# Kernel optimization log

Measured on AMD Instinct MI355X. Metric: run time of the kernel, lower is better.

## Reference

```python
import jax, jax.numpy as jnp
import numpy as np

B, N, IN, OUT, H = 256, 131, 512, 1024, 4
D = OUT // H  # head_dim
EDGE_SCALE = D ** -0.5
NODE_SCALE = OUT ** -0.5

lrelu = lambda x: jax.nn.leaky_relu(x, negative_slope=0.01)


def _glorot(key, shape):
    fan_in = shape[-1]
    return jax.random.normal(key, shape, dtype=jnp.float32) * (1.0 / np.sqrt(fan_in))


def setup_inputs() -> dict:
    key = jax.random.key(0)
    ks = jax.random.split(key, 16)
    return {
        "tabular_feats": jax.random.normal(ks[0], (B, 1, IN), dtype=jnp.float32),
        "node_feats": jax.random.normal(ks[1], (B, N, IN), dtype=jnp.float32),
        "adj_matrix": jax.random.uniform(ks[2], (B, N, N), dtype=jnp.float32),
        "W_gx": _glorot(ks[3], (OUT, IN)), "b_gx": jnp.zeros((OUT,), jnp.float32),
        "W_tx": _glorot(ks[4], (OUT, IN)), "b_tx": jnp.zeros((OUT,), jnp.float32),
        "W_gk": _glorot(ks[5], (OUT, IN)),
        "W_tq": _glorot(ks[6], (OUT, IN)),
        "W_gq": _glorot(ks[7], (OUT, IN)),
        "W_gs": _glorot(ks[8], (1, N)), "b_gs": jnp.zeros((1,), jnp.float32),
        "W_zx": _glorot(ks[9], (OUT, 2 * OUT)), "b_zx": jnp.zeros((OUT,), jnp.float32),
    }


def preprocess_adj(A):
    # add self-loops then symmetric degree normalization D^{-1/2} (A+I) D^{-1/2}
    A = A + jnp.eye(A.shape[-1], dtype=A.dtype)
    d_inv = jax.lax.rsqrt(jnp.sum(A, axis=-1))  # [b,h,x]
    return d_inv[..., :, None] * A * d_inv[..., None, :]


def reference(tabular_feats, node_feats, adj_matrix,
              W_gx, b_gx, W_tx, b_tx, W_gk, W_tq, W_gq, W_gs, b_gs, W_zx, b_zx):
    G_X = lrelu(node_feats @ W_gx.T + b_gx)            # [B,N,OUT]
    T_X = lrelu(tabular_feats @ W_tx.T + b_tx)         # [B,1,OUT]
    G_k = lrelu(node_feats @ W_gk.T)                   # [B,N,OUT]
    T_q = lrelu(tabular_feats @ W_tq.T)                # [B,1,OUT]

    node_att = jax.nn.softmax(jnp.einsum('bxh,byh->bxy', T_q, G_k) * NODE_SCALE, axis=-1)
    node_att = jnp.swapaxes(node_att + 1.0, -1, -2)    # [B,N,1]
    G_X = node_att * G_X                               # [B,N,OUT]

    G_X_mh = G_X.reshape(B, N, H, D).transpose(0, 2, 1, 3)            # [B,H,N,D]
    G_q_mh = lrelu(node_feats @ W_gq.T).reshape(B, N, H, D).transpose(0, 2, 1, 3)
    G_k_mh = G_k.reshape(B, N, H, D).transpose(0, 2, 1, 3)

    edge_att = jax.nn.sigmoid(jnp.einsum('bhxd,bhyd->bhxy', G_q_mh, G_k_mh) * EDGE_SCALE)
    adj_heads = adj_matrix[:, None] * edge_att         # [B,H,N,N]
    A = preprocess_adj(adj_heads)

    G_X = jnp.einsum('bhxy,bhyd->bhxd', A, G_X_mh).transpose(0, 2, 1, 3).reshape(B, N, OUT)

    # Graph_summary: Linear(num_node -> 1) over the node axis
    global_node = lrelu(jnp.einsum('bno,n->bo', G_X, W_gs[0]) + b_gs)  # [B,OUT]
    Z_in = jnp.concatenate([global_node, T_X.reshape(B, -1)], axis=-1)  # [B,2*OUT]
    Z_x = lrelu(Z_in @ W_zx.T + b_zx)                  # [B,OUT]
    return (G_X, T_X, Z_x, node_att, edge_att)
```

## Files before the change

kernel.cpp:

```cpp
#include <hip/hip_runtime.h>
#include <hip/hip_bf16.h>
#include <math.h>


#define LRELU(x) ((x) > 0.f ? (x) : 0.01f * (x))

constexpr int Bb = 256;
constexpr int Nn = 131;
constexpr int INF_ = 512;
constexpr int OUTF = 1024;
constexpr int Hh = 4;
constexpr int Dd = 256;
constexpr int OC2 = 2048;
constexpr int YP = 168;
constexpr int WLP = 174;
constexpr int KAGG = 160;

typedef __attribute__((ext_vector_type(8))) short bf16x8;
typedef __attribute__((ext_vector_type(4))) float f32x4;

__device__ __forceinline__ float bf2f(short s) {
    union { float f; unsigned u; } c;
    c.u = ((unsigned)(unsigned short)s) << 16;
    return c.f;
}

__device__ __forceinline__ void gload_lds16(const void* g, void* lds) {
    __builtin_amdgcn_global_load_lds(
        (const __attribute__((address_space(1))) void*)g,
        (__attribute__((address_space(3))) void*)lds, 16, 0, 0);
}

__global__ __launch_bounds__(256) void convert_kernel(
    const float* __restrict__ node, const float* __restrict__ Wgx,
    const float* __restrict__ Wgk, const float* __restrict__ Wgq,
    __hip_bfloat16* __restrict__ node_bf, __hip_bfloat16* __restrict__ Wcat)
{
    const size_t NE = (size_t)Bb * Nn * INF_ / 4;
    const size_t WE = (size_t)3072 * INF_ / 4;
    for (size_t i = (size_t)blockIdx.x * 256 + threadIdx.x; i < NE + WE;
         i += (size_t)gridDim.x * 256) {
        if (i < NE) {
            const float4 v = ((const float4*)node)[i];
            __hip_bfloat16* o = node_bf + i * 4;
            o[0] = __float2bfloat16(v.x); o[1] = __float2bfloat16(v.y);
            o[2] = __float2bfloat16(v.z); o[3] = __float2bfloat16(v.w);
        } else {
            const size_t j = i - NE;
            const size_t which = j / (1024 * INF_ / 4);
            const float* src = (which == 0) ? Wgk : (which == 1 ? Wgq : Wgx);
            const size_t srcj = j - which * (1024 * INF_ / 4);
            const float4 v = ((const float4*)src)[srcj];
            __hip_bfloat16* o = Wcat + j * 4;
            o[0] = __float2bfloat16(v.x); o[1] = __float2bfloat16(v.y);
            o[2] = __float2bfloat16(v.z); o[3] = __float2bfloat16(v.w);
        }
    }
}

__global__ __launch_bounds__(256, 4) void gemm_node_mfma(
    const __hip_bfloat16* __restrict__ A, const __hip_bfloat16* __restrict__ W,
    const float* __restrict__ bias_gx, const float* __restrict__ Tq,
    __hip_bfloat16* __restrict__ Gcat, __hip_bfloat16* __restrict__ GrawT,
    float* __restrict__ spart)
{
    __shared__ short SM[16384];
    short* As = SM;
    short* Bs = SM + 8192;
    const int tid = threadIdx.x;
    const int wave = tid >> 6, lane = tid & 63;
    const int m0 = blockIdx.y * 128, o0 = blockIdx.x * 128;
    const int wr = wave >> 1, wc = wave & 1;

    f32x4 acc[4][4] = {};
    const short* Asrc = (const short*)A;
    const short* Wsrc = (const short*)W;
    const int gsrc = ((tid & 7) ^ ((tid >> 3) & 7)) * 8;
    const int srow = tid >> 3;

    for (int kt = 0; kt < 8; ++kt) {
        const int k0 = kt * 64;
        #pragma unroll
        for (int j = 0; j < 4; ++j) {
            const int row = j * 32 + srow;
            gload_lds16(Asrc + (size_t)(m0 + row) * INF_ + k0 + gsrc,
                        &As[(j * 256 + (tid & ~63)) * 8]);
            gload_lds16(Wsrc + (size_t)(o0 + row) * INF_ + k0 + gsrc,
                        &Bs[(j * 256 + (tid & ~63)) * 8]);
        }
        __syncthreads();
        #pragma unroll
        for (int ks = 0; ks < 2; ++ks) {
            const int sa = ((ks * 4 + (lane >> 4)) ^ (lane & 7)) * 8;
            bf16x8 af[4], bfr[4];
            #pragma unroll
            for (int i = 0; i < 4; ++i) {
                af[i]  = *(const bf16x8*)&As[(wr * 64 + i * 16 + (lane & 15)) * 64 + sa];
                bfr[i] = *(const bf16x8*)&Bs[(wc * 64 + i * 16 + (lane & 15)) * 64 + sa];
            }
            #pragma unroll
            for (int mi = 0; mi < 4; ++mi)
                #pragma unroll
                for (int ni = 0; ni < 4; ++ni)
                    acc[mi][ni] = __builtin_amdgcn_mfma_f32_16x16x32_bf16(
                        af[mi], bfr[ni], acc[mi][ni], 0, 0, 0);
        }
        __syncthreads();
    }

    const int cc = lane & 15;
    const int rg = (lane >> 4) * 4;
    if (o0 < 1024) {
        const int blo = m0 / 131;
        const int msw = (blo + 1) * 131;
        float tqA[4], tqB[4];
        #pragma unroll
        for (int ni = 0; ni < 4; ++ni) {
            const int o = o0 + wc * 64 + ni * 16 + cc;
            tqA[ni] = Tq[(size_t)blo * OUTF + o];
            tqB[ni] = (blo + 1 < Bb) ? Tq[(size_t)(blo + 1) * OUTF + o] : 0.f;
        }
        float sc[4][4] = {};
        #pragma unroll
        for (int mi = 0; mi < 4; ++mi)
            #pragma unroll
            for (int ni = 0; ni < 4; ++ni) {
                const int o = o0 + wc * 64 + ni * 16 + cc;
                #pragma unroll
                for (int r = 0; r < 4; ++r) {
                    const int m = m0 + wr * 64 + mi * 16 + rg + r;
                    float v = acc[mi][ni][r];
                    v = LRELU(v);
                    Gcat[(size_t)m * OC2 + o] = __float2bfloat16(v);
                    sc[mi][r] += v * ((m >= msw) ? tqB[ni] : tqA[ni]);
                }
            }
        const int slot = (o0 >> 6) + wc;
        #pragma unroll
        for (int mi = 0; mi < 4; ++mi)
            #pragma unroll
            for (int r = 0; r < 4; ++r) {
                float s = sc[mi][r];
                s += __shfl_xor(s, 1); s += __shfl_xor(s, 2);
                s += __shfl_xor(s, 4); s += __shfl_xor(s, 8);
                if (cc == 0) {
                    const int m = m0 + wr * 64 + mi * 16 + rg + r;
                    spart[(size_t)m * 16 + slot] = s;
                }
            }
    } else if (o0 < OC2) {
        #pragma unroll
        for (int mi = 0; mi < 4; ++mi)
            #pragma unroll
            for (int ni = 0; ni < 4; ++ni) {
                const int o = o0 + wc * 64 + ni * 16 + cc;
                #pragma unroll
                for (int r = 0; r < 4; ++r) {
                    const int m = m0 + wr * 64 + mi * 16 + rg + r;
                    float v = acc[mi][ni][r];
                    v = LRELU(v);
                    Gcat[(size_t)m * OC2 + o] = __float2bfloat16(v);
                }
            }
    } else {
        const int og0 = o0 - OC2;
        const int h = og0 >> 8;
        const int dbase = og0 & 255;
        __syncthreads();
        #pragma unroll
        for (int mi = 0; mi < 4; ++mi)
            #pragma unroll
            for (int ni = 0; ni < 4; ++ni) {
                const int dloc = wc * 64 + ni * 16 + cc;
                const float badd = bias_gx[og0 + dloc];
                #pragma unroll
                for (int r = 0; r < 4; ++r) {
                    const int row = wr * 64 + mi * 16 + rg + r;
                    float v = acc[mi][ni][r] + badd;
                    v = LRELU(v);
                    __hip_bfloat16 hb = __float2bfloat16(v);
                    const int g = row >> 3;
                    SM[dloc * 128 + ((g ^ (dloc & 7)) << 3) + (row & 7)] = *(short*)&hb;
                }
            }
        __syncthreads();
        short* GT = (short*)GrawT;
        #pragma unroll
        for (int j = 0; j < 8; ++j) {
            const int task = j * 256 + tid;
            const int dloc = task >> 4;
            const int g = task & 15;
            const bf16x8 v = *(const bf16x8*)&SM[dloc * 128 + ((g ^ (dloc & 7)) << 3)];
            const int m = m0 + g * 8;
            const int gd = dbase + dloc;
            const int b0 = m / 131;
            const int n0 = m - b0 * 131;
            if (n0 + 8 <= Nn) {
                *(bf16x8*)&GT[((size_t)(b0 * Hh + h) * 256 + gd) * YP + n0] = v;
            } else {
                #pragma unroll
                for (int e = 0; e < 8; ++e) {
                    const int mm = m + e;
                    const int bb = mm / 131;
                    const int nn = mm - bb * 131;
                    GT[((size_t)(bb * Hh + h) * 256 + gd) * YP + nn] = ((const short*)&v)[e];
                }
            }
        }
    }
}

__global__ __launch_bounds__(256) void gemm_tab(
    const float* __restrict__ Atab, const float* __restrict__ Wtx,
    const float* __restrict__ btx, const float* __restrict__ Wtq,
    float* __restrict__ Ctx, float* __restrict__ Ctq)
{
    const int which = blockIdx.x >> 4;
    const float* Wm = which ? Wtq : Wtx;
    float* C = which ? Ctq : Ctx;
    __shared__ float As[16][68];
    __shared__ float Ws[16][68];
    const int tid = threadIdx.x;
    const int tx = tid & 15;
    const int ty = tid >> 4;
    const int m0 = blockIdx.y * 64;
    const int o0 = (blockIdx.x & 15) * 64;

    float acc[4][4] = {};
    for (int k0 = 0; k0 < INF_; k0 += 16) {
        const int j = tid & 15;
        const int i = tid >> 4;
        #pragma unroll
        for (int r = 0; r < 4; ++r)
            As[j][i + 16 * r] = Atab[(size_t)(m0 + i + 16 * r) * INF_ + k0 + j];
        #pragma unroll
        for (int r = 0; r < 4; ++r)
            Ws[j][i + 16 * r] = Wm[(size_t)(o0 + i + 16 * r) * INF_ + k0 + j];
        __syncthreads();
        #pragma unroll
        for (int kk = 0; kk < 16; ++kk) {
            const float4 av = *(const float4*)&As[kk][ty * 4];
            const float4 wv = *(const float4*)&Ws[kk][tx * 4];
            const float a[4] = {av.x, av.y, av.z, av.w};
            const float w[4] = {wv.x, wv.y, wv.z, wv.w};
            #pragma unroll
            for (int r = 0; r < 4; ++r)
                #pragma unroll
                for (int c = 0; c < 4; ++c)
                    acc[r][c] += a[r] * w[c];
        }
        __syncthreads();
    }
    #pragma unroll
    for (int r = 0; r < 4; ++r) {
        const int m = m0 + ty * 4 + r;
        const int o = o0 + tx * 4;
        float4 v;
        float* vp = (float*)&v;
        #pragma unroll
        for (int c = 0; c < 4; ++c) {
            float t = acc[r][c] + (which ? 0.f : btx[o + c]);
            vp[c] = LRELU(t);
        }
        *(float4*)&C[(size_t)m * OUTF + o] = v;
    }
}

__global__ __launch_bounds__(256) void zin_build(
    const float* __restrict__ gnode, const float* __restrict__ bgs,
    const float* __restrict__ Tx, float* __restrict__ Zin)
{
    const int idx = blockIdx.x * 256 + threadIdx.x;
    const int b = idx >> 10, o = idx & 1023;
    const float s = gnode[idx] + bgs[0];
    Zin[(size_t)b * 2048 + o] = LRELU(s);
    Zin[(size_t)b * 2048 + 1024 + o] = Tx[idx];
}

__global__ __launch_bounds__(256) void gemm_zsplit(
    const float* __restrict__ A, const float* __restrict__ W,
    float* __restrict__ P)
{
    __shared__ float As[16][68];
    __shared__ float Ws[16][68];
    const int tid = threadIdx.x;
    const int tx = tid & 15;
    const int ty = tid >> 4;
    const int m0 = blockIdx.y * 64;
    const int o0 = blockIdx.x * 64;
    const int kbase = blockIdx.z * 512;

    float acc[4][4] = {};
    for (int k0 = kbase; k0 < kbase + 512; k0 += 16) {
        const int j = tid & 15;
        const int i = tid >> 4;
        #pragma unroll
        for (int r = 0; r < 4; ++r)
            As[j][i + 16 * r] = A[(size_t)(m0 + i + 16 * r) * 2048 + k0 + j];
        #pragma unroll
        for (int r = 0; r < 4; ++r)
            Ws[j][i + 16 * r] = W[(size_t)(o0 + i + 16 * r) * 2048 + k0 + j];
        __syncthreads();
        #pragma unroll
        for (int kk = 0; kk < 16; ++kk) {
            const float4 av = *(const float4*)&As[kk][ty * 4];
            const float4 wv = *(const float4*)&Ws[kk][tx * 4];
            const float a[4] = {av.x, av.y, av.z, av.w};
            const float w[4] = {wv.x, wv.y, wv.z, wv.w};
            #pragma unroll
            for (int r = 0; r < 4; ++r)
                #pragma unroll
                for (int c = 0; c < 4; ++c)
                    acc[r][c] += a[r] * w[c];
        }
        __syncthreads();
    }
    float* pz = P + (size_t)blockIdx.z * Bb * OUTF;
    #pragma unroll
    for (int r = 0; r < 4; ++r) {
        const int m = m0 + ty * 4 + r;
        const int o = o0 + tx * 4;
        float4 v;
        float* vp = (float*)&v;
        #pragma unroll
        for (int c = 0; c < 4; ++c) vp[c] = acc[r][c];
        *(float4*)&pz[(size_t)m * OUTF + o] = v;
    }
}

__global__ __launch_bounds__(256) void zreduce(
    const float* __restrict__ P, const float* __restrict__ bzx,
    float* __restrict__ C)
{
    const int idx = blockIdx.x * 256 + threadIdx.x;
    const int o = idx & 1023;
    const size_t STRIDE = (size_t)Bb * OUTF;
    float s = P[idx] + P[STRIDE + idx] + P[2 * STRIDE + idx] + P[3 * STRIDE + idx]
            + bzx[o];
    C[idx] = LRELU(s);
}

__global__ __launch_bounds__(256) void nodeatt_soft(
    const float* __restrict__ spart, float* __restrict__ att)
{
    const int b = blockIdx.x;
    __shared__ float sc[136];
    const int tid = threadIdx.x;
    if (tid < Nn) {
        const float* sp = spart + (size_t)(b * Nn + tid) * 16;
        float s = 0.f;
        #pragma unroll
        for (int i = 0; i < 16; ++i) s += sp[i];
        sc[tid] = s * (1.f / 32.f);
    }
    __syncthreads();
    if (tid < 64) {
        const float v1 = sc[tid];
        const float v2 = sc[tid + 64];
        const float v3 = (tid < 3) ? sc[tid + 128] : -1e30f;
        float m = fmaxf(fmaxf(v1, v2), v3);
        #pragma unroll
        for (int off = 32; off; off >>= 1) m = fmaxf(m, __shfl_xor(m, off));
        const float e1 = expf(v1 - m);
        const float e2 = expf(v2 - m);
        const float e3 = (tid < 3) ? expf(v3 - m) : 0.f;
        float s = e1 + e2 + e3;
        #pragma unroll
        for (int off = 32; off; off >>= 1) s += __shfl_xor(s, off);
        const float inv = 1.f / s;
        float* ab = att + (size_t)b * Nn;
        ab[tid] = e1 * inv + 1.f;
        ab[tid + 64] = e2 * inv + 1.f;
        if (tid < 3) ab[tid + 128] = e3 * inv + 1.f;
    }
}

__global__ __launch_bounds__(576) void edge_agg(
    const __hip_bfloat16* __restrict__ Gcat, const float* __restrict__ adj,
    const float* __restrict__ att, const __hip_bfloat16* __restrict__ GrawT,
    const float* __restrict__ Wgs, float* __restrict__ edge,
    float* __restrict__ Gout, float* __restrict__ gnode)
{
    __shared__ short SM[25056];
    __shared__ float rsL[144 * 3];
    __shared__ float dxL[Nn], daL[Nn], attL[Nn], wgsL[Nn];

    const int bh = blockIdx.x, b = bh >> 2, h = bh & 3;
    const int tid = threadIdx.x;
    const int lane = tid & 63, wid = tid >> 6;
    const int wr = wid / 3, wc = wid % 3;
    if (tid < Nn) { attL[tid] = att[(size_t)b * Nn + tid]; wgsL[tid] = Wgs[tid]; }

    const short* qb = (const short*)Gcat + (size_t)b * Nn * OC2 + 1024 + h * Dd;
    const short* kb = (const short*)Gcat + (size_t)b * Nn * OC2 + h * Dd;
    const short* gsrcT = (const short*)GrawT + (size_t)bh * 256 * YP;

    int srow = tid >> 2; if (srow > Nn - 1) srow = Nn - 1;
    const int gsrc = ((tid & 3) ^ ((tid >> 3) & 3)) * 8;
    const int dstoff = (tid & ~63) * 8;

    auto STAGE = [&](int buf, int k0) {
        gload_lds16(qb + (size_t)srow * OC2 + k0 + gsrc, &SM[buf * 4608 + dstoff]);
        gload_lds16(kb + (size_t)srow * OC2 + k0 + gsrc, &SM[9216 + buf * 4608 + dstoff]);
    };

    f32x4 acc[3][3] = {};
    const int sa = ((lane >> 4) ^ ((lane >> 1) & 3)) * 8;

    STAGE(0, 0);
    for (int t = 0; t < 8; ++t) {
        const int buf = t & 1;
        if (t < 7) {
            STAGE(buf ^ 1, (t + 1) * 32);
            asm volatile("s_waitcnt vmcnt(2)" ::: "memory");
        } else {
            asm volatile("s_waitcnt vmcnt(0)" ::: "memory");
        }
        __builtin_amdgcn_s_barrier();
        __builtin_amdgcn_sched_barrier(0);
        bf16x8 qf[3], kf[3];
        #pragma unroll
        for (int i = 0; i < 3; ++i) {
            qf[i] = *(const bf16x8*)&SM[buf * 4608 + (wr * 48 + i * 16 + (lane & 15)) * 32 + sa];
            kf[i] = *(const bf16x8*)&SM[9216 + buf * 4608 + (wc * 48 + i * 16 + (lane & 15)) * 32 + sa];
        }
        __builtin_amdgcn_s_setprio(1);
        #pragma unroll
        for (int mi = 0; mi < 3; ++mi)
            #pragma unroll
            for (int ni = 0; ni < 3; ++ni)
                acc[mi][ni] = __builtin_amdgcn_mfma_f32_16x16x32_bf16(
                    qf[mi], kf[ni], acc[mi][ni], 0, 0, 0);
        __builtin_amdgcn_s_setprio(0);
        __builtin_amdgcn_sched_barrier(0);
        if (t < 7) __builtin_amdgcn_s_barrier();
    }

    const float* adjb = adj + (size_t)b * Nn * Nn;
    float* edgeb = edge + (size_t)bh * Nn * Nn;
    const int cc = lane & 15;
    const int rg = (lane >> 4) * 4;
    float areg[3][3][4];
    #pragma unroll
    for (int mi = 0; mi < 3; ++mi) {
        float rsum[4] = {0.f, 0.f, 0.f, 0.f};
        #pragma unroll
        for (int ni = 0; ni < 3; ++ni) {
            const int y = wc * 48 + ni * 16 + cc;
            #pragma unroll
            for (int r = 0; r < 4; ++r) {
                const int x = wr * 48 + mi * 16 + rg + r;
                const bool in = (x < Nn) && (y < Nn);
                const float a = in ? adjb[x * Nn + y] : 0.f;
                areg[mi][ni][r] = a;
                const float e = 1.f / (1.f + __expf(-acc[mi][ni][r] * (1.f / 16.f)));
                acc[mi][ni][r] = e;
                if (in) {
                    edgeb[x * Nn + y] = e;
                    rsum[r] += a * e;
                }
            }
        }
        #pragma unroll
        for (int r = 0; r < 4; ++r) {
            float v = rsum[r];
            v += __shfl_xor(v, 1); v += __shfl_xor(v, 2);
            v += __shfl_xor(v, 4); v += __shfl_xor(v, 8);
            const int x = wr * 48 + mi * 16 + rg + r;
            if (cc == 0 && x < Nn) rsL[x * 3 + wc] = v;
        }
    }
    __syncthreads();
    if (tid < Nn) {
        const float s = rsL[tid * 3] + rsL[tid * 3 + 1] + rsL[tid * 3 + 2];
        const float dv = rsqrtf(s + 1.f);
        dxL[tid] = dv;
        daL[tid] = dv * attL[tid];
    }
    __syncthreads();

    const int brow0 = wid * 32 + (lane & 15);
    const int bcol = (lane >> 4) * 8;
    bf16x8 bcur0, bcur1;
    if (wid < 8) {
        bcur0 = *(const bf16x8*)&gsrcT[(size_t)brow0 * YP + 0 + bcol];
        bcur1 = *(const bf16x8*)&gsrcT[(size_t)(brow0 + 16) * YP + 0 + bcol];
    }

    short* WbL = SM;
    for (int i = tid; i < 144 * 29; i += 576) {
        const int x = i / 29, y = 131 + i % 29;
        WbL[x * WLP + y] = 0;
    }
    #pragma unroll
    for (int mi = 0; mi < 3; ++mi)
        #pragma unroll
        for (int ni = 0; ni < 3; ++ni) {
            const int y = wc * 48 + ni * 16 + cc;
            #pragma unroll
            for (int r = 0; r < 4; ++r) {
                const int x = wr * 48 + mi * 16 + rg + r;
                if (x < Nn && y < Nn) {
                    float a = areg[mi][ni][r] * acc[mi][ni][r];
                    if (x == y) a += 1.f;
                    const float w = dxL[x] * a * daL[y];
                    __hip_bfloat16 hb = __float2bfloat16(w);
                    WbL[(size_t)x * WLP + y] = *(short*)&hb;
                }
            }
        }
    __syncthreads();

    if (wid < 8) {
        f32x4 gacc[9][2] = {};
        #pragma unroll
        for (int kc = 0; kc < 5; ++kc) {
            bf16x8 bnxt0, bnxt1;
            if (kc < 4) {
                bnxt0 = *(const bf16x8*)&gsrcT[(size_t)brow0 * YP + (kc + 1) * 32 + bcol];
                bnxt1 = *(const bf16x8*)&gsrcT[(size_t)(brow0 + 16) * YP + (kc + 1) * 32 + bcol];
            }
            bf16x8 af[9];
            #pragma unroll
            for (int mi = 0; mi < 9; ++mi)
                af[mi] = *(const bf16x8*)&WbL[(mi * 16 + (lane & 15)) * WLP + kc * 32 + (lane >> 4) * 8];
            __builtin_amdgcn_s_setprio(1);
            #pragma unroll
            for (int mi = 0; mi < 9; ++mi) {
                gacc[mi][0] = __builtin_amdgcn_mfma_f32_16x16x32_bf16(
                    af[mi], bcur0, gacc[mi][0], 0, 0, 0);
                gacc[mi][1] = __builtin_amdgcn_mfma_f32_16x16x32_bf16(
                    af[mi], bcur1, gacc[mi][1], 0, 0, 0);
            }
            __builtin_amdgcn_s_setprio(0);
            if (kc < 4) { bcur0 = bnxt0; bcur1 = bnxt1; }
        }

        float* gob = Gout + (size_t)b * Nn * OUTF + h * Dd;
        float gp[2] = {0.f, 0.f};
        #pragma unroll
        for (int mi = 0; mi < 9; ++mi)
            #pragma unroll
            for (int ni = 0; ni < 2; ++ni) {
                const int d = wid * 32 + ni * 16 + (lane & 15);
                #pragma unroll
                for (int r = 0; r < 4; ++r) {
                    const int x = mi * 16 + (lane >> 4) * 4 + r;
                    if (x < Nn) {
                        gob[(size_t)x * OUTF + d] = gacc[mi][ni][r];
                        gp[ni] += wgsL[x] * gacc[mi][ni][r];
                    }
                }
            }
        #pragma unroll
        for (int ni = 0; ni < 2; ++ni) {
            gp[ni] += __shfl_xor(gp[ni], 16);
            gp[ni] += __shfl_xor(gp[ni], 32);
            if (lane < 16)
                gnode[(size_t)b * OUTF + h * Dd + wid * 32 + ni * 16 + lane] = gp[ni];
        }
    }
}

extern "C" void kernel_launch(void* const* d_in, const int* in_sizes, int n_in,
                              void* d_out, int out_size, void* d_ws, size_t ws_size,
                              hipStream_t stream) {
    const float* tab  = (const float*)d_in[0];
    const float* node = (const float*)d_in[1];
    const float* adj  = (const float*)d_in[2];
    const float* W_gx = (const float*)d_in[3];
    const float* b_gx = (const float*)d_in[4];
    const float* W_tx = (const float*)d_in[5];
    const float* b_tx = (const float*)d_in[6];
    const float* W_gk = (const float*)d_in[7];
    const float* W_tq = (const float*)d_in[8];
    const float* W_gq = (const float*)d_in[9];
    const float* W_gs = (const float*)d_in[10];
    const float* b_gs = (const float*)d_in[11];
    const float* W_zx = (const float*)d_in[12];
    const float* b_zx = (const float*)d_in[13];

    const size_t GX_ELEMS = (size_t)Bb * Nn * OUTF;
    const int M_NODE = Bb * Nn;

    float* out   = (float*)d_out;
    float* o_GX  = out;
    float* o_TX  = o_GX + GX_ELEMS;
    float* o_ZX  = o_TX + (size_t)Bb * OUTF;
    float* o_ATT = o_ZX + (size_t)Bb * OUTF;
    float* o_EDG = o_ATT + (size_t)Bb * Nn;

    __hip_bfloat16* wb      = (__hip_bfloat16*)d_ws;
    __hip_bfloat16* w_nodeb = wb;
    __hip_bfloat16* w_Wcat  = w_nodeb + (size_t)M_NODE * INF_;
    __hip_bfloat16* w_Gcat  = w_Wcat + (size_t)3072 * INF_;
    __hip_bfloat16* w_GrawT = w_Gcat + (size_t)M_NODE * OC2;
    float* wf       = (float*)(w_GrawT + (size_t)Bb * Hh * 256 * YP);
    float* w_Tq     = wf;
    float* w_Zin    = w_Tq + (size_t)Bb * OUTF;
    float* w_gnode  = w_Zin + (size_t)Bb * 2 * OUTF;
    float* w_spart  = w_gnode + (size_t)Bb * OUTF;
    float* w_zpart  = w_spart + (size_t)M_NODE * 16;

    const dim3 blk(256);

    convert_kernel<<<dim3(2048), blk, 0, stream>>>(node, W_gx, W_gk, W_gq,
                                                   w_nodeb, w_Wcat);
    gemm_tab<<<dim3(32, 4), blk, 0, stream>>>(tab, W_tx, b_tx, W_tq, o_TX, w_Tq);
    gemm_node_mfma<<<dim3(24, M_NODE / 128), blk, 0, stream>>>(
        w_nodeb, w_Wcat, b_gx, w_Tq, w_Gcat, w_GrawT, w_spart);
    nodeatt_soft<<<dim3(Bb), blk, 0, stream>>>(w_spart, o_ATT);
    edge_agg<<<dim3(Bb * Hh), dim3(576), 0, stream>>>(
        w_Gcat, adj, o_ATT, w_GrawT, W_gs, o_EDG, o_GX, w_gnode);
    zin_build<<<dim3((Bb * OUTF) / 256), blk, 0, stream>>>(w_gnode, b_gs, o_TX, w_Zin);
    gemm_zsplit<<<dim3(16, 4, 4), blk, 0, stream>>>(w_Zin, W_zx, w_zpart);
    zreduce<<<dim3((Bb * OUTF) / 256), blk, 0, stream>>>(w_zpart, b_zx, o_ZX);
}
```

Measured before the change: 389.3 us.

## Cut edge_agg register pressure by staging edge values in LDS

Replaces the per-thread areg array and in-register sigmoid values with a bf16 copy staged in shared memory, and reloads adjacency from global memory in the second pass. The aggregation GEMM now processes its two column tiles one after another with a non-unrolled k-loop, halving the live accumulator set and dropping the register double-buffering of B fragments. A min-blocks hint of 5 is added to launch_bounds to push the compiler toward fewer VGPRs and higher occupancy. The cost is extra LDS traffic, a second adj read, an extra barrier, loss of load/compute overlap, and the edge weight now being rounded to bf16 before it is combined with adj.

```diff
diff --git a/kernel.cpp b/kernel.cpp
--- a/kernel.cpp
+++ b/kernel.cpp
@@ -375,7 +375,7 @@
     }
 }
 
-__global__ __launch_bounds__(576) void edge_agg(
+__global__ __launch_bounds__(576, 5) void edge_agg(
     const __hip_bfloat16* __restrict__ Gcat, const float* __restrict__ adj,
     const float* __restrict__ att, const __hip_bfloat16* __restrict__ GrawT,
     const float* __restrict__ Wgs, float* __restrict__ edge,
@@ -435,12 +435,13 @@
         __builtin_amdgcn_sched_barrier(0);
         if (t < 7) __builtin_amdgcn_s_barrier();
     }
+    __syncthreads();
 
     const float* adjb = adj + (size_t)b * Nn * Nn;
     float* edgeb = edge + (size_t)bh * Nn * Nn;
     const int cc = lane & 15;
     const int rg = (lane >> 4) * 4;
-    float areg[3][3][4];
+    short* eL = SM;
     #pragma unroll
     for (int mi = 0; mi < 3; ++mi) {
         float rsum[4] = {0.f, 0.f, 0.f, 0.f};
@@ -451,14 +452,15 @@
             for (int r = 0; r < 4; ++r) {
                 const int x = wr * 48 + mi * 16 + rg + r;
                 const bool in = (x < Nn) && (y < Nn);
-                const float a = in ? adjb[x * Nn + y] : 0.f;
-                areg[mi][ni][r] = a;
                 const float e = 1.f / (1.f + __expf(-acc[mi][ni][r] * (1.f / 16.f)));
-                acc[mi][ni][r] = e;
+                float ew = 0.f;
                 if (in) {
                     edgeb[x * Nn + y] = e;
-                    rsum[r] += a * e;
-                }
+                    rsum[r] += adjb[x * Nn + y] * e;
+                    ew = e;
+                }
+                __hip_bfloat16 he = __float2bfloat16(ew);
+                eL[x * WLP + y] = *(short*)&he;
             }
         }
         #pragma unroll
@@ -470,6 +472,10 @@
             if (cc == 0 && x < Nn) rsL[x * 3 + wc] = v;
         }
     }
+    for (int i = tid; i < 144 * 16; i += 576) {
+        const int x = i >> 4, y = 144 + (i & 15);
+        eL[x * WLP + y] = 0;
+    }
     __syncthreads();
     if (tid < Nn) {
         const float s = rsL[tid * 3] + rsL[tid * 3 + 1] + rsL[tid * 3 + 2];
@@ -479,19 +485,6 @@
     }
     __syncthreads();
 
-    const int brow0 = wid * 32 + (lane & 15);
-    const int bcol = (lane >> 4) * 8;
-    bf16x8 bcur0, bcur1;
-    if (wid < 8) {
-        bcur0 = *(const bf16x8*)&gsrcT[(size_t)brow0 * YP + 0 + bcol];
-        bcur1 = *(const bf16x8*)&gsrcT[(size_t)(brow0 + 16) * YP + 0 + bcol];
-    }
-
-    short* WbL = SM;
-    for (int i = tid; i < 144 * 29; i += 576) {
-        const int x = i / 29, y = 131 + i % 29;
-        WbL[x * WLP + y] = 0;
-    }
     #pragma unroll
     for (int mi = 0; mi < 3; ++mi)
         #pragma unroll
@@ -500,64 +493,56 @@
             #pragma unroll
             for (int r = 0; r < 4; ++r) {
                 const int x = wr * 48 + mi * 16 + rg + r;
+                float w = 0.f;
                 if (x < Nn && y < Nn) {
-                    float a = areg[mi][ni][r] * acc[mi][ni][r];
+                    float a = adjb[x * Nn + y] * bf2f(eL[x * WLP + y]);
                     if (x == y) a += 1.f;
-                    const float w = dxL[x] * a * daL[y];
-                    __hip_bfloat16 hb = __float2bfloat16(w);
-                    WbL[(size_t)x * WLP + y] = *(short*)&hb;
-                }
+                    w = dxL[x] * a * daL[y];
+                }
+                __hip_bfloat16 hb = __float2bfloat16(w);
+                eL[x * WLP + y] = *(short*)&hb;
             }
         }
     __syncthreads();
 
+    const short* WbL = SM;
     if (wid < 8) {
-        f32x4 gacc[9][2] = {};
-        #pragma unroll
-        for (int kc = 0; kc < 5; ++kc) {
-            bf16x8 bnxt0, bnxt1;
-            if (kc < 4) {
-                bnxt0 = *(const bf16x8*)&gsrcT[(size_t)brow0 * YP + (kc + 1) * 32 + bcol];
-                bnxt1 = *(const bf16x8*)&gsrcT[(size_t)(brow0 + 16) * YP + (kc + 1) * 32 + bcol];
-            }
-            bf16x8 af[9];
+        float* gob = Gout + (size_t)b * Nn * OUTF + h * Dd;
+        const int bcol = (lane >> 4) * 8;
+        #pragma unroll
+        for (int ni = 0; ni < 2; ++ni) {
+            const int brow = wid * 32 + ni * 16 + (lane & 15);
+            f32x4 gacc[9] = {};
+            #pragma unroll 1
+            for (int kc = 0; kc < 5; ++kc) {
+                const bf16x8 bfr = *(const bf16x8*)&gsrcT[(size_t)brow * YP + kc * 32 + bcol];
+                bf16x8 af[9];
+                #pragma unroll
+                for (int mi = 0; mi < 9; ++mi)
+                    af[mi] = *(const bf16x8*)&WbL[(mi * 16 + (lane & 15)) * WLP + kc * 32 + (lane >> 4) * 8];
+                __builtin_amdgcn_s_setprio(1);
+                #pragma unroll
+                for (int mi = 0; mi < 9; ++mi)
+                    gacc[mi] = __builtin_amdgcn_mfma_f32_16x16x32_bf16(
+                        af[mi], bfr, gacc[mi], 0, 0, 0);
+                __builtin_amdgcn_s_setprio(0);
+            }
+            const int d = wid * 32 + ni * 16 + (lane & 15);
+            float gp = 0.f;
             #pragma unroll
             for (int mi = 0; mi < 9; ++mi)
-                af[mi] = *(const bf16x8*)&WbL[(mi * 16 + (lane & 15)) * WLP + kc * 32 + (lane >> 4) * 8];
-            __builtin_amdgcn_s_setprio(1);
-            #pragma unroll
-            for (int mi = 0; mi < 9; ++mi) {
-                gacc[mi][0] = __builtin_amdgcn_mfma_f32_16x16x32_bf16(
-                    af[mi], bcur0, gacc[mi][0], 0, 0, 0);
-                gacc[mi][1] = __builtin_amdgcn_mfma_f32_16x16x32_bf16(
-                    af[mi], bcur1, gacc[mi][1], 0, 0, 0);
-            }
-            __builtin_amdgcn_s_setprio(0);
-            if (kc < 4) { bcur0 = bnxt0; bcur1 = bnxt1; }
-        }
-
-        float* gob = Gout + (size_t)b * Nn * OUTF + h * Dd;
-        float gp[2] = {0.f, 0.f};
-        #pragma unroll
-        for (int mi = 0; mi < 9; ++mi)
-            #pragma unroll
-            for (int ni = 0; ni < 2; ++ni) {
-                const int d = wid * 32 + ni * 16 + (lane & 15);
                 #pragma unroll
                 for (int r = 0; r < 4; ++r) {
                     const int x = mi * 16 + (lane >> 4) * 4 + r;
                     if (x < Nn) {
-                        gob[(size_t)x * OUTF + d] = gacc[mi][ni][r];
-                        gp[ni] += wgsL[x] * gacc[mi][ni][r];
+                        gob[(size_t)x * OUTF + d] = gacc[mi][r];
+                        gp += wgsL[x] * gacc[mi][r];
                     }
                 }
-            }
-        #pragma unroll
-        for (int ni = 0; ni < 2; ++ni) {
-            gp[ni] += __shfl_xor(gp[ni], 16);
-            gp[ni] += __shfl_xor(gp[ni], 32);
+            gp += __shfl_xor(gp, 16);
+            gp += __shfl_xor(gp, 32);
             if (lane < 16)
-                gnode[(size_t)b * OUTF + h * Dd + wid * 32 + ni * 16 + lane] = gp[ni];
+                gnode[(size_t)b * OUTF + h * Dd + d] = gp;
         }
     }
 }
```

Result: slower. 450.2 us (+15.7%).
